# Kernel tuning notes

Measured on AMD Instinct MI355X. Metric: run time of the kernel, lower is better.

Reference implementation:

```python
import jax, jax.numpy as jnp
import numpy as np
import math

DIM = 512
HEADS = 16
HD = DIM // HEADS
HT, WT = 32, 32          # trained input_resolution
LT = HT * WT             # trained_len
TBL = (2 * HT - 1) * (2 * WT - 1)  # 3969 rows in relative_coords_table
CPB_HID = 512


def _l2norm(a, eps=1e-12):
    n = jnp.linalg.norm(a, axis=-1, keepdims=True)
    return a / jnp.maximum(n, eps)


def setup_inputs() -> dict:
    key = jax.random.key(0)
    ks = jax.random.split(key, 10)
    B, N = 8, 1024
    std = 0.02
    return {
        "x": jax.random.normal(ks[0], (B, N, DIM), jnp.float32),
        "qkv_w": jax.random.normal(ks[1], (3 * DIM, DIM), jnp.float32) * std,
        "qkv_b": jnp.zeros((3 * DIM,), jnp.float32),
        "proj_w": jax.random.normal(ks[2], (DIM, DIM), jnp.float32) * std,
        "proj_b": jnp.zeros((DIM,), jnp.float32),
        # softplus-inverse init: softplus(temperature) == 1/0.24
        "temperature": jnp.log(jnp.exp(jnp.ones((HEADS, 1, 1), jnp.float32) / 0.24) - 1.0),
        "query_embedding": jax.random.normal(ks[3], (HEADS, 1, HD), jnp.float32) * 0.02,
        "cpb_fc1_w": jax.random.normal(ks[4], (CPB_HID, 2), jnp.float32) * std,
        "cpb_fc1_b": jnp.zeros((CPB_HID,), jnp.float32),
        "cpb_fc2_w": jax.random.normal(ks[5], (HEADS, CPB_HID), jnp.float32) * std,
        "cpb_fc2_b": jnp.zeros((HEADS,), jnp.float32),
        "relative_coords_table": jax.random.uniform(ks[6], (TBL, 2), jnp.float32, -1.0, 1.0),
        "relative_pos_index": jax.random.randint(ks[7], (LT * LT,), 0, TBL, jnp.int32),
        "seq_length_scale": jnp.float32(math.log(float(N))),
        "padding_mask": jnp.zeros((B, N), bool),
        "H": 32,
        "W": 32,
    }


def reference(x, qkv_w, qkv_b, proj_w, proj_b, temperature, query_embedding,
              cpb_fc1_w, cpb_fc1_b, cpb_fc2_w, cpb_fc2_b,
              relative_coords_table, seq_length_scale,
              relative_pos_index, padding_mask, H, W):
    B, N, C = x.shape
    # qkv projection -> [B, N, 3, heads, hd] -> per-tensor [B, heads, N, hd]
    qkv = (x @ qkv_w.T + qkv_b).reshape(B, N, 3, HEADS, HD)
    q, k, v = (jnp.transpose(qkv[:, :, i], (0, 2, 1, 3)) for i in range(3))

    # continuous position bias MLP: [TBL, 2] -> [TBL, heads]
    t = jnp.maximum(relative_coords_table @ cpb_fc1_w.T + cpb_fc1_b, 0.0)
    t = t @ cpb_fc2_w.T + cpb_fc2_b                       # [TBL, heads]
    rb = t.T[:, relative_pos_index]                       # [heads, LT*LT]
    rb = rb.reshape(HEADS, LT, HT, WT)
    rb = jax.image.resize(rb, (HEADS, LT, H, W), 'bilinear')   # interp key axis
    rb = rb.reshape(HEADS, LT, N).transpose(0, 2, 1).reshape(HEADS, N, HT, WT)
    rb = jax.image.resize(rb, (HEADS, N, H, W), 'bilinear')    # interp query axis
    rb = rb.reshape(HEADS, N, N).transpose(0, 2, 1)             # [heads, N, N]

    scale = jax.nn.softplus(temperature) * seq_length_scale     # [heads, 1, 1]
    qn = (_l2norm(q) + query_embedding[None]) * scale[None]     # [B, heads, N, hd]
    kn = _l2norm(k)
    attn = jnp.einsum('bhnd,bhmd->bhnm', qn, kn) + rb[None]     # [B, heads, N, N]
    attn = jax.nn.softmax(attn, axis=-1)
    out = jnp.einsum('bhnm,bhmd->bhnd', attn, v)
    out = out.transpose(0, 2, 1, 3).reshape(B, N, C)
    return out @ proj_w.T + proj_b
```

## Files before the change

### kernel.cpp

```cpp
#include <hip/hip_runtime.h>
#include <math.h>

#define BATCH 8
#define NSEQ  1024
#define DIMC  512
#define HEADS 16
#define HD    32
#define TBLN  3969
#define QROWS (BATCH*HEADS*NSEQ)
#define LOG2E 1.4426950408889634f

typedef __attribute__((ext_vector_type(8))) short bf16x8;
typedef __attribute__((ext_vector_type(4))) float f32x4;

__device__ __forceinline__ unsigned short f2bf(float f) {
  union { float f; unsigned u; } c; c.f = f;
  unsigned x = c.u + 0x7fffu + ((c.u >> 16) & 1u);
  return (unsigned short)(x >> 16);
}
__device__ __forceinline__ float bf2f(unsigned short h) {
  union { unsigned u; float f; } c; c.u = ((unsigned)h) << 16; return c.f;
}
__device__ __forceinline__ unsigned cvt_pk_bf16(float lo, float hi) {
  unsigned r;
  asm("v_cvt_pk_bf16_f32 %0, %1, %2" : "=v"(r) : "v"(lo), "v"(hi));
  return r;
}

#define GLD(gsrc, ldst) __builtin_amdgcn_global_load_lds( \
      (const __attribute__((address_space(1))) unsigned int*)(gsrc), \
      (__attribute__((address_space(3))) unsigned int*)(ldst), 16, 0, 0)

__global__ __launch_bounds__(256) void split_kernel(
    const float* __restrict__ src, unsigned short* __restrict__ hi,
    unsigned short* __restrict__ lo, int n4)
{
  int gid = blockIdx.x * 256 + threadIdx.x;
  if (gid >= n4) return;
  float4 v = ((const float4*)src)[gid];
  float vv[4] = {v.x, v.y, v.z, v.w};
  unsigned short h[4], l[4];
#pragma unroll
  for (int i = 0; i < 4; ++i) {
    h[i] = f2bf(vv[i]);
    l[i] = f2bf(vv[i] - bf2f(h[i]));
  }
  uint2 hp, lp;
  hp.x = h[0] | ((unsigned)h[1] << 16); hp.y = h[2] | ((unsigned)h[3] << 16);
  lp.x = l[0] | ((unsigned)l[1] << 16); lp.y = l[2] | ((unsigned)l[3] << 16);
  ((uint2*)hi)[gid] = hp;
  ((uint2*)lo)[gid] = lp;
}

template<int EPI>
__global__ __launch_bounds__(256) void gemm_split_kernel(
    const unsigned short* __restrict__ Ah, const unsigned short* __restrict__ Al,
    const unsigned short* __restrict__ Wh, const unsigned short* __restrict__ Wl,
    const float* __restrict__ bias,
    float* __restrict__ o0p, float* __restrict__ o1p, float* __restrict__ o2p)
{
  const int K = DIMC;
  __shared__ __align__(16) unsigned short lds[4 * 4096];
  unsigned short* ldsAh = lds;
  unsigned short* ldsAl = lds + 4096;
  unsigned short* ldsBh = lds + 8192;
  unsigned short* ldsBl = lds + 12288;
  const int tid = threadIdx.x;
  const int wave = tid >> 6, lane = tid & 63;
  const int l16 = lane & 15, hi4 = lane >> 4;
  const int rowBase = blockIdx.y * 128, colBase = blockIdx.x * 128;
  const int warpRow = (wave >> 1) * 64, warpCol = (wave & 1) * 64;

  const int o0 = wave * 2048 + lane * 16;
  const int o1 = o0 + 1024;
  const int row0 = o0 >> 6, s0 = (o0 >> 4) & 3;
  const int row1 = o1 >> 6, s1 = (o1 >> 4) & 3;
  const int g0 = row0 * K + ((s0 ^ ((row0 >> 1) & 3)) << 3);
  const int g1 = row1 * K + ((s1 ^ ((row1 >> 1) & 3)) << 3);

  const unsigned short* A0h = Ah + (size_t)rowBase * K;
  const unsigned short* A0l = Al + (size_t)rowBase * K;
  const unsigned short* W0h = Wh + (size_t)colBase * K;
  const unsigned short* W0l = Wl + (size_t)colBase * K;

  f32x4 acc[4][4] = {};

  float biasv[4];
#pragma unroll
  for (int fj = 0; fj < 4; ++fj)
    biasv[fj] = bias[colBase + warpCol + fj * 16 + l16];

  int ra[4], rbq[4];
#pragma unroll
  for (int f = 0; f < 4; ++f) {
    int rowA = warpRow + f * 16 + l16;
    ra[f] = rowA * 64 + ((hi4 ^ ((rowA >> 1) & 3)) << 4);
    int rowB = warpCol + f * 16 + l16;
    rbq[f] = rowB * 64 + ((hi4 ^ ((rowB >> 1) & 3)) << 4);
  }

  for (int k0 = 0; k0 < K; k0 += 32) {
    __syncthreads();
    GLD(A0h + k0 + g0, (char*)ldsAh + o0);
    GLD(A0h + k0 + g1, (char*)ldsAh + o1);
    GLD(A0l + k0 + g0, (char*)ldsAl + o0);
    GLD(A0l + k0 + g1, (char*)ldsAl + o1);
    GLD(W0h + k0 + g0, (char*)ldsBh + o0);
    GLD(W0h + k0 + g1, (char*)ldsBh + o1);
    GLD(W0l + k0 + g0, (char*)ldsBl + o0);
    GLD(W0l + k0 + g1, (char*)ldsBl + o1);
    __syncthreads();

    bf16x8 a_h[4], a_l[4], b_h[4], b_l[4];
#pragma unroll
    for (int f = 0; f < 4; ++f) {
      a_h[f] = *(const bf16x8*)((const char*)ldsAh + ra[f]);
      a_l[f] = *(const bf16x8*)((const char*)ldsAl + ra[f]);
      b_h[f] = *(const bf16x8*)((const char*)ldsBh + rbq[f]);
      b_l[f] = *(const bf16x8*)((const char*)ldsBl + rbq[f]);
    }
#pragma unroll
    for (int fi = 0; fi < 4; ++fi)
#pragma unroll
      for (int fj = 0; fj < 4; ++fj) {
        acc[fi][fj] = __builtin_amdgcn_mfma_f32_16x16x32_bf16(a_l[fi], b_h[fj], acc[fi][fj], 0, 0, 0);
        acc[fi][fj] = __builtin_amdgcn_mfma_f32_16x16x32_bf16(a_h[fi], b_l[fj], acc[fi][fj], 0, 0, 0);
        acc[fi][fj] = __builtin_amdgcn_mfma_f32_16x16x32_bf16(a_h[fi], b_h[fj], acc[fi][fj], 0, 0, 0);
      }
  }

#pragma unroll
  for (int fi = 0; fi < 4; ++fi)
#pragma unroll
    for (int fj = 0; fj < 4; ++fj)
#pragma unroll
      for (int r = 0; r < 4; ++r) {
        int m = rowBase + warpRow + fi * 16 + hi4 * 4 + r;
        int c = colBase + warpCol + fj * 16 + l16;
        float val = acc[fi][fj][r] + biasv[fj];
        if (EPI == 0) {
          int b = m >> 10, n = m & 1023;
          int which = c >> 9, rem = c & 511;
          int hh = rem >> 5, d = rem & 31;
          float* dst = (which == 0) ? o0p : (which == 1) ? o1p : o2p;
          dst[(((size_t)b * HEADS + hh) * NSEQ + n) * HD + d] = val;
        } else {
          o0p[(size_t)m * DIMC + c] = val;
        }
      }
}

__global__ __launch_bounds__(256) void cpb_kernel(
    const float* __restrict__ table, const float* __restrict__ fc1w,
    const float* __restrict__ fc1b, const float* __restrict__ fc2w,
    const float* __restrict__ fc2b, float* __restrict__ tT)
{
  const int row = blockIdx.x;
  const float c0 = table[row*2], c1 = table[row*2+1];
  __shared__ float hid[512];
  __shared__ float red[256];
  const int tid = threadIdx.x;
  for (int j = tid; j < 512; j += 256)
    hid[j] = fmaxf(fmaf(c0, fc1w[j*2], fmaf(c1, fc1w[j*2+1], fc1b[j])), 0.f);
  __syncthreads();
  const int h = tid & 15, part = tid >> 4;
  float s = 0.f;
#pragma unroll
  for (int jj = 0; jj < 32; ++jj) {
    int j = part*32 + jj;
    s = fmaf(hid[j], fc2w[h*512 + j], s);
  }
  red[tid] = s;
  __syncthreads();
  if (tid < 16) {
    float t = fc2b[tid];
#pragma unroll
    for (int p = 0; p < 16; ++p) t += red[tid + p*16];
    tT[(size_t)tid * TBLN + row] = t;
  }
}

__global__ __launch_bounds__(256) void rb_gather_kernel(
    const float* __restrict__ tT, const int* __restrict__ rpi,
    unsigned short* __restrict__ rbT)
{
  int gid = blockIdx.x * 256 + threadIdx.x;
  int n = gid >> 7, m8 = gid & 127;
  int idx[8];
#pragma unroll
  for (int j = 0; j < 8; ++j) idx[j] = rpi[(size_t)n * NSEQ + m8 * 8 + j];
  const int kt = m8 >> 2, hi4v = m8 & 3;
  const size_t base = (((size_t)0 * 64 + (n >> 4)) * 32 + kt) * 512
                      + ((n & 15) + 16 * hi4v) * 8;
#pragma unroll
  for (int h = 0; h < 16; ++h) {
    bf16x8 v;
#pragma unroll
    for (int j = 0; j < 8; ++j)
      v[j] = (short)f2bf(tT[h * TBLN + idx[j]] * LOG2E);
    *(bf16x8*)(rbT + base + (size_t)h * 64 * 32 * 512) = v;
  }
}

__global__ __launch_bounds__(256) void rowmax_kernel(
    const unsigned short* __restrict__ rbT, float* __restrict__ rbmax)
{
  const int row = blockIdx.x * 4 + (threadIdx.x >> 6);
  const int lane = threadIdx.x & 63;
  const int h = row >> 10, n = row & 1023;
  const int kt = lane >> 1, half = lane & 1;
  const size_t base = (((size_t)h * 64 + (n >> 4)) * 32 + kt) * 512;
  bf16x8 a = *(const bf16x8*)(rbT + base + ((n & 15) + 16 * (2 * half)) * 8);
  bf16x8 b = *(const bf16x8*)(rbT + base + ((n & 15) + 16 * (2 * half + 1)) * 8);
  float m = -1e30f;
#pragma unroll
  for (int j = 0; j < 8; ++j) {
    m = fmaxf(m, bf2f((unsigned short)a[j]));
    m = fmaxf(m, bf2f((unsigned short)b[j]));
  }
#pragma unroll
  for (int s = 32; s >= 1; s >>= 1) m = fmaxf(m, __shfl_xor(m, s));
  if (lane == 0) rbmax[row] = m;
}

__global__ __launch_bounds__(256) void normsplit_kernel(
    const float* __restrict__ qb, const float* __restrict__ kb,
    const float* __restrict__ temperature, const float* __restrict__ qe,
    const float* __restrict__ sls,
    unsigned short* __restrict__ qh, unsigned short* __restrict__ ql,
    unsigned short* __restrict__ khT, unsigned short* __restrict__ klT,
    float* __restrict__ qmag)
{
  const int gid = blockIdx.x * 256 + threadIdx.x;
  const int lane = gid & 31;
  const int row = gid >> 5;
  const bool isQ = row < QROWS;
  const float* src = isQ ? qb : kb;
  const int r = isQ ? row : row - QROWS;
  float x = src[(size_t)r * HD + lane];
  float ss = x * x;
#pragma unroll
  for (int m = 16; m >= 1; m >>= 1) ss += __shfl_xor(ss, m);
  float y = x / fmaxf(sqrtf(ss), 1e-12f);
  if (isQ) {
    const int h = (r >> 10) & (HEADS - 1);
    float scale = log1pf(__expf(temperature[h])) * sls[0];
    y = (y + qe[h * HD + lane]) * scale;
    float s2 = y * y;
#pragma unroll
    for (int m = 16; m >= 1; m >>= 1) s2 += __shfl_xor(s2, m);
    if (lane == 0) qmag[r] = sqrtf(s2);
  }
  unsigned short hi = f2bf(y);
  unsigned short lo = f2bf(y - bf2f(hi));
  if (isQ) {
    size_t idx = (size_t)r * HD + lane;
    qh[idx] = hi; ql[idx] = lo;
  } else {
    const int bh = r >> 10, n = r & 1023;
    const int kt = n >> 5, kr = n & 31;
    const int s = (kr >> 2) & 1;
    const int l16v = 4 * (kr >> 3) + (kr & 3);
    size_t idx = ((((size_t)bh * 32 + kt) * 2 + s) * 512)
                 + (l16v + 16 * (lane >> 3)) * 8 + (lane & 7);
    khT[idx] = hi; klT[idx] = lo;
  }
}

__global__ __launch_bounds__(256) void vt_kernel(
    const float* __restrict__ vb, unsigned short* __restrict__ vtT)
{
  __shared__ float tile[32][257];
  const int bh = blockIdx.x, ch = blockIdx.y;
  const int t = threadIdx.x;
  const float* src = vb + ((size_t)bh * NSEQ + ch * 256) * HD;
#pragma unroll
  for (int i = 0; i < 32; ++i) {
    int idx = i * 256 + t;
    tile[idx & 31][idx >> 5] = src[idx];
  }
  __syncthreads();
  unsigned short* dst = vtT + (size_t)bh * 32 * 2 * 512;
#pragma unroll
  for (int i = 0; i < 32; ++i) {
    int idx = i * 256 + t;
    int d = idx >> 8, nl = idx & 255;
    int n = ch * 256 + nl;
    size_t a = (((size_t)(n >> 5) * 2) + (d >> 4)) * 512
               + ((d & 15) + 16 * ((n >> 3) & 3)) * 8 + (n & 7);
    dst[a] = f2bf(tile[d][nl]);
  }
}

__global__ __launch_bounds__(256, 6) void attn_mfma_kernel(
    const unsigned short* __restrict__ qh, const unsigned short* __restrict__ ql,
    const unsigned short* __restrict__ khT, const unsigned short* __restrict__ klT,
    const unsigned short* __restrict__ vtT, const unsigned short* __restrict__ rbT,
    const float* __restrict__ qmag, const float* __restrict__ rbmax,
    unsigned short* __restrict__ aoh, unsigned short* __restrict__ aol)
{
  const int bh = blockIdx.x;
  const int h = bh & (HEADS - 1), b = bh >> 4;
  const int wave = threadIdx.x >> 6;
  const int lane = threadIdx.x & 63;
  const int l16 = lane & 15, hi4 = lane >> 4;
  const int qbase = blockIdx.y * 64 + wave * 16;

  const int qrow = qbase + l16;
  bf16x8 qhf, qlf;
  {
    size_t ro = ((size_t)bh * NSEQ + qrow) * HD + hi4 * 8;
    qhf = *(const bf16x8*)(qh + ro);
    qlf = *(const bf16x8*)(ql + ro);
  }
  const float Ms = qmag[(size_t)bh * NSEQ + qrow] * (1.01f * LOG2E)
                   + rbmax[h * NSEQ + qrow] + 0.2f;

  bf16x8 ones;
#pragma unroll
  for (int j = 0; j < 8; ++j) ones[j] = (short)0x3f80;

  f32x4 accV0 = {}, accV1 = {}, accL = {};

  const unsigned short* khB = khT + (size_t)bh * 32768 + lane * 8;
  const unsigned short* klB = klT + (size_t)bh * 32768 + lane * 8;
  const unsigned short* vtB = vtT + (size_t)bh * 32768 + lane * 8;
  const unsigned short* rbB = rbT
      + ((size_t)(h * 64 + blockIdx.y * 4 + wave) * 32) * 512 + lane * 8;

  for (int kt = 0; kt < 32; ++kt) {
    bf16x8 kh0 = *(const bf16x8*)(khB + kt * 1024);
    bf16x8 kh1 = *(const bf16x8*)(khB + kt * 1024 + 512);
    bf16x8 kl0 = *(const bf16x8*)(klB + kt * 1024);
    bf16x8 kl1 = *(const bf16x8*)(klB + kt * 1024 + 512);
    bf16x8 vt0 = *(const bf16x8*)(vtB + kt * 1024);
    bf16x8 vt1 = *(const bf16x8*)(vtB + kt * 1024 + 512);
    bf16x8 b8  = *(const bf16x8*)(rbB + kt * 512);

    f32x4 D0 = {0.f, 0.f, 0.f, 0.f};
    f32x4 D1 = {0.f, 0.f, 0.f, 0.f};
    __builtin_amdgcn_s_setprio(1);
    D0 = __builtin_amdgcn_mfma_f32_16x16x32_bf16(kh0, qhf, D0, 0, 0, 0);
    D0 = __builtin_amdgcn_mfma_f32_16x16x32_bf16(kh0, qlf, D0, 0, 0, 0);
    D0 = __builtin_amdgcn_mfma_f32_16x16x32_bf16(kl0, qhf, D0, 0, 0, 0);
    D1 = __builtin_amdgcn_mfma_f32_16x16x32_bf16(kh1, qhf, D1, 0, 0, 0);
    D1 = __builtin_amdgcn_mfma_f32_16x16x32_bf16(kh1, qlf, D1, 0, 0, 0);
    D1 = __builtin_amdgcn_mfma_f32_16x16x32_bf16(kl1, qhf, D1, 0, 0, 0);
    __builtin_amdgcn_s_setprio(0);

    float p0[4], p1[4];
#pragma unroll
    for (int r = 0; r < 4; ++r) {
      float a0 = fmaf(D0[r], LOG2E, bf2f((unsigned short)b8[r]))     - Ms;
      float a1 = fmaf(D1[r], LOG2E, bf2f((unsigned short)b8[4 + r])) - Ms;
      p0[r] = __builtin_amdgcn_exp2f(a0);
      p1[r] = __builtin_amdgcn_exp2f(a1);
    }
    union { bf16x8 v; unsigned u[4]; } pa;
    pa.u[0] = cvt_pk_bf16(p0[0], p0[1]);
    pa.u[1] = cvt_pk_bf16(p0[2], p0[3]);
    pa.u[2] = cvt_pk_bf16(p1[0], p1[1]);
    pa.u[3] = cvt_pk_bf16(p1[2], p1[3]);

    __builtin_amdgcn_s_setprio(1);
    accV0 = __builtin_amdgcn_mfma_f32_16x16x32_bf16(pa.v, vt0, accV0, 0, 0, 0);
    accV1 = __builtin_amdgcn_mfma_f32_16x16x32_bf16(pa.v, vt1, accV1, 0, 0, 0);
    accL  = __builtin_amdgcn_mfma_f32_16x16x32_bf16(pa.v, ones, accL, 0, 0, 0);
    __builtin_amdgcn_s_setprio(0);
  }

#pragma unroll
  for (int r = 0; r < 4; ++r) {
    float inv = 1.f / accL[r];
#pragma unroll
    for (int df = 0; df < 2; ++df) {
      size_t idx = ((size_t)b * NSEQ + qbase + hi4 * 4 + r) * DIMC
                   + h * HD + df * 16 + l16;
      float val = (df ? accV1[r] : accV0[r]) * inv;
      unsigned short hh = f2bf(val);
      aoh[idx] = hh;
      aol[idx] = f2bf(val - bf2f(hh));
    }
  }
}

extern "C" void kernel_launch(void* const* d_in, const int* in_sizes, int n_in,
                              void* d_out, int out_size, void* d_ws, size_t ws_size,
                              hipStream_t stream)
{
  (void)in_sizes; (void)n_in; (void)out_size; (void)ws_size;
  const float* x      = (const float*)d_in[0];
  const float* qkv_w  = (const float*)d_in[1];
  const float* qkv_b  = (const float*)d_in[2];
  const float* proj_w = (const float*)d_in[3];
  const float* proj_b = (const float*)d_in[4];
  const float* temp   = (const float*)d_in[5];
  const float* qe     = (const float*)d_in[6];
  const float* fc1w   = (const float*)d_in[7];
  const float* fc1b   = (const float*)d_in[8];
  const float* fc2w   = (const float*)d_in[9];
  const float* fc2b   = (const float*)d_in[10];
  const float* tbl    = (const float*)d_in[11];
  const int*   rpi    = (const int*)d_in[12];
  const float* sls    = (const float*)d_in[13];

  char* ws = (char*)d_ws;
  const size_t perT = (size_t)BATCH * HEADS * NSEQ * HD;
  float* qb = (float*)ws;
  float* kb = qb + perT;
  float* vb = kb + perT;
  float* tT = vb + perT;
  unsigned short* qh = (unsigned short*)(tT + 65536);
  unsigned short* ql = qh + perT;
  unsigned short* khT = ql + perT;
  unsigned short* klT = khT + perT;
  unsigned short* vtT = klT + perT;
  unsigned short* xh = vtT + perT;
  unsigned short* xl = xh + perT;
  unsigned short* pwh = xl + perT;
  unsigned short* pwl = pwh + 262144;
  float* rbmax = (float*)(pwl + 262144);
  float* qmag  = rbmax + 16384;
  unsigned short* qwh = qh;
  unsigned short* qwl = qh + 786432;
  unsigned short* rbT = (unsigned short*)qb;
  unsigned short* aoh = xh;
  unsigned short* aol = xl;

  split_kernel<<<dim3(4096), 256, 0, stream>>>(x, xh, xl, 1048576);
  split_kernel<<<dim3(768),  256, 0, stream>>>(qkv_w, qwh, qwl, 196608);
  split_kernel<<<dim3(256),  256, 0, stream>>>(proj_w, pwh, pwl, 65536);
  gemm_split_kernel<0><<<dim3(12, 64), 256, 0, stream>>>(
      xh, xl, qwh, qwl, qkv_b, qb, kb, vb);
  cpb_kernel<<<dim3(TBLN), 256, 0, stream>>>(tbl, fc1w, fc1b, fc2w, fc2b, tT);
  normsplit_kernel<<<dim3((2*QROWS*32)/256), 256, 0, stream>>>(
      qb, kb, temp, qe, sls, qh, ql, khT, klT, qmag);
  vt_kernel<<<dim3(BATCH*HEADS, NSEQ/256), 256, 0, stream>>>(vb, vtT);
  rb_gather_kernel<<<dim3((NSEQ*NSEQ/8)/256), 256, 0, stream>>>(tT, rpi, rbT);
  rowmax_kernel<<<dim3(HEADS*NSEQ/4), 256, 0, stream>>>(rbT, rbmax);
  attn_mfma_kernel<<<dim3(BATCH*HEADS, NSEQ/64), 256, 0, stream>>>(
      qh, ql, khT, klT, vtT, rbT, qmag, rbmax, aoh, aol);
  gemm_split_kernel<1><<<dim3(4, 64), 256, 0, stream>>>(
      aoh, aol, pwh, pwl, proj_b, (float*)d_out, nullptr, nullptr);
}
```

Measured before the change: 353.7 us.

## Fuse V transpose/bf16 pack into QKV GEMM epilogue; shrink proj GEMM tile

```diff
diff --git a/kernel.cpp b/kernel.cpp
--- a/kernel.cpp
+++ b/kernel.cpp
@@ -52,75 +52,93 @@
   ((uint2*)lo)[gid] = lp;
 }
 
-template<int EPI>
+template<int EPI, int BM>
 __global__ __launch_bounds__(256) void gemm_split_kernel(
     const unsigned short* __restrict__ Ah, const unsigned short* __restrict__ Al,
     const unsigned short* __restrict__ Wh, const unsigned short* __restrict__ Wl,
     const float* __restrict__ bias,
-    float* __restrict__ o0p, float* __restrict__ o1p, float* __restrict__ o2p)
+    float* __restrict__ o0p, float* __restrict__ o1p,
+    unsigned short* __restrict__ vtp)
 {
   const int K = DIMC;
-  __shared__ __align__(16) unsigned short lds[4 * 4096];
+  constexpr int ASZ = BM * 32;
+  constexpr int FI  = BM / 32;
+  __shared__ __align__(16) unsigned short lds[2 * ASZ + 8192];
   unsigned short* ldsAh = lds;
-  unsigned short* ldsAl = lds + 4096;
-  unsigned short* ldsBh = lds + 8192;
-  unsigned short* ldsBl = lds + 12288;
+  unsigned short* ldsAl = lds + ASZ;
+  unsigned short* ldsBh = lds + 2 * ASZ;
+  unsigned short* ldsBl = lds + 2 * ASZ + 4096;
   const int tid = threadIdx.x;
   const int wave = tid >> 6, lane = tid & 63;
   const int l16 = lane & 15, hi4 = lane >> 4;
-  const int rowBase = blockIdx.y * 128, colBase = blockIdx.x * 128;
-  const int warpRow = (wave >> 1) * 64, warpCol = (wave & 1) * 64;
-
-  const int o0 = wave * 2048 + lane * 16;
-  const int o1 = o0 + 1024;
-  const int row0 = o0 >> 6, s0 = (o0 >> 4) & 3;
-  const int row1 = o1 >> 6, s1 = (o1 >> 4) & 3;
-  const int g0 = row0 * K + ((s0 ^ ((row0 >> 1) & 3)) << 3);
-  const int g1 = row1 * K + ((s1 ^ ((row1 >> 1) & 3)) << 3);
+  const int rowBase = blockIdx.y * BM, colBase = blockIdx.x * 128;
+  const int warpRow = (wave >> 1) * (BM / 2), warpCol = (wave & 1) * 64;
+
+  const int oB0 = wave * 2048 + lane * 16;
+  const int oB1 = oB0 + 1024;
+  const int rB0 = oB0 >> 6, sB0 = (oB0 >> 4) & 3;
+  const int rB1 = oB1 >> 6, sB1 = (oB1 >> 4) & 3;
+  const int gB0 = rB0 * K + ((sB0 ^ ((rB0 >> 1) & 3)) << 3);
+  const int gB1 = rB1 * K + ((sB1 ^ ((rB1 >> 1) & 3)) << 3);
+  const int oA0 = (BM == 128) ? (wave * 2048 + lane * 16)
+                              : (wave * 1024 + lane * 16);
+  const int oA1 = oA0 + 1024;
+  const int rA0 = oA0 >> 6, sA0 = (oA0 >> 4) & 3;
+  const int rA1 = oA1 >> 6, sA1 = (oA1 >> 4) & 3;
+  const int gA0 = rA0 * K + ((sA0 ^ ((rA0 >> 1) & 3)) << 3);
+  const int gA1 = rA1 * K + ((sA1 ^ ((rA1 >> 1) & 3)) << 3);
 
   const unsigned short* A0h = Ah + (size_t)rowBase * K;
   const unsigned short* A0l = Al + (size_t)rowBase * K;
   const unsigned short* W0h = Wh + (size_t)colBase * K;
   const unsigned short* W0l = Wl + (size_t)colBase * K;
 
-  f32x4 acc[4][4] = {};
+  f32x4 acc[FI][4] = {};
 
   float biasv[4];
 #pragma unroll
   for (int fj = 0; fj < 4; ++fj)
     biasv[fj] = bias[colBase + warpCol + fj * 16 + l16];
 
-  int ra[4], rbq[4];
-#pragma unroll
-  for (int f = 0; f < 4; ++f) {
+  int ra[FI], rbq[4];
+#pragma unroll
+  for (int f = 0; f < FI; ++f) {
     int rowA = warpRow + f * 16 + l16;
     ra[f] = rowA * 64 + ((hi4 ^ ((rowA >> 1) & 3)) << 4);
+  }
+#pragma unroll
+  for (int f = 0; f < 4; ++f) {
     int rowB = warpCol + f * 16 + l16;
     rbq[f] = rowB * 64 + ((hi4 ^ ((rowB >> 1) & 3)) << 4);
   }
 
   for (int k0 = 0; k0 < K; k0 += 32) {
     __syncthreads();
-    GLD(A0h + k0 + g0, (char*)ldsAh + o0);
-    GLD(A0h + k0 + g1, (char*)ldsAh + o1);
-    GLD(A0l + k0 + g0, (char*)ldsAl + o0);
-    GLD(A0l + k0 + g1, (char*)ldsAl + o1);
-    GLD(W0h + k0 + g0, (char*)ldsBh + o0);
-    GLD(W0h + k0 + g1, (char*)ldsBh + o1);
-    GLD(W0l + k0 + g0, (char*)ldsBl + o0);
-    GLD(W0l + k0 + g1, (char*)ldsBl + o1);
+    GLD(A0h + k0 + gA0, (char*)ldsAh + oA0);
+    GLD(A0l + k0 + gA0, (char*)ldsAl + oA0);
+    if constexpr (BM == 128) {
+      GLD(A0h + k0 + gA1, (char*)ldsAh + oA1);
+      GLD(A0l + k0 + gA1, (char*)ldsAl + oA1);
+    }
+    GLD(W0h + k0 + gB0, (char*)ldsBh + oB0);
+    GLD(W0h + k0 + gB1, (char*)ldsBh + oB1);
+    GLD(W0l + k0 + gB0, (char*)ldsBl + oB0);
+    GLD(W0l + k0 + gB1, (char*)ldsBl + oB1);
     __syncthreads();
 
-    bf16x8 a_h[4], a_l[4], b_h[4], b_l[4];
-#pragma unroll
-    for (int f = 0; f < 4; ++f) {
+    bf16x8 a_h[FI], a_l[FI], b_h[4], b_l[4];
+#pragma unroll
+    for (int f = 0; f < FI; ++f) {
       a_h[f] = *(const bf16x8*)((const char*)ldsAh + ra[f]);
       a_l[f] = *(const bf16x8*)((const char*)ldsAl + ra[f]);
+    }
+#pragma unroll
+    for (int f = 0; f < 4; ++f) {
       b_h[f] = *(const bf16x8*)((const char*)ldsBh + rbq[f]);
       b_l[f] = *(const bf16x8*)((const char*)ldsBl + rbq[f]);
     }
 #pragma unroll
-    for (int fi = 0; fi < 4; ++fi)
+    for (int fi = 0; fi < FI; ++fi)
 #pragma unroll
       for (int fj = 0; fj < 4; ++fj) {
         acc[fi][fj] = __builtin_amdgcn_mfma_f32_16x16x32_bf16(a_l[fi], b_h[fj], acc[fi][fj], 0, 0, 0);
@@ -130,7 +148,7 @@
   }
 
 #pragma unroll
-  for (int fi = 0; fi < 4; ++fi)
+  for (int fi = 0; fi < FI; ++fi)
 #pragma unroll
     for (int fj = 0; fj < 4; ++fj)
 #pragma unroll
@@ -142,8 +160,16 @@
           int b = m >> 10, n = m & 1023;
           int which = c >> 9, rem = c & 511;
           int hh = rem >> 5, d = rem & 31;
-          float* dst = (which == 0) ? o0p : (which == 1) ? o1p : o2p;
-          dst[(((size_t)b * HEADS + hh) * NSEQ + n) * HD + d] = val;
+          if (which == 2) {
+            int bh = b * HEADS + hh;
+            size_t a = (size_t)bh * 32768
+                     + (size_t)(n >> 5) * 1024 + (size_t)(d >> 4) * 512
+                     + ((d & 15) + 16 * ((n >> 3) & 3)) * 8 + (n & 7);
+            vtp[a] = f2bf(val);
+          } else {
+            float* dst = (which == 0) ? o0p : o1p;
+            dst[(((size_t)b * HEADS + hh) * NSEQ + n) * HD + d] = val;
+          }
         } else {
           o0p[(size_t)m * DIMC + c] = val;
         }
@@ -264,31 +290,6 @@
     size_t idx = ((((size_t)bh * 32 + kt) * 2 + s) * 512)
                  + (l16v + 16 * (lane >> 3)) * 8 + (lane & 7);
     khT[idx] = hi; klT[idx] = lo;
-  }
-}
-
-__global__ __launch_bounds__(256) void vt_kernel(
-    const float* __restrict__ vb, unsigned short* __restrict__ vtT)
-{
-  __shared__ float tile[32][257];
-  const int bh = blockIdx.x, ch = blockIdx.y;
-  const int t = threadIdx.x;
-  const float* src = vb + ((size_t)bh * NSEQ + ch * 256) * HD;
-#pragma unroll
-  for (int i = 0; i < 32; ++i) {
-    int idx = i * 256 + t;
-    tile[idx & 31][idx >> 5] = src[idx];
-  }
-  __syncthreads();
-  unsigned short* dst = vtT + (size_t)bh * 32 * 2 * 512;
-#pragma unroll
-  for (int i = 0; i < 32; ++i) {
-    int idx = i * 256 + t;
-    int d = idx >> 8, nl = idx & 255;
-    int n = ch * 256 + nl;
-    size_t a = (((size_t)(n >> 5) * 2) + (d >> 4)) * 512
-               + ((d & 15) + 16 * ((n >> 3) & 3)) * 8 + (n & 7);
-    dst[a] = f2bf(tile[d][nl]);
   }
 }
 
@@ -430,16 +431,15 @@
   split_kernel<<<dim3(4096), 256, 0, stream>>>(x, xh, xl, 1048576);
   split_kernel<<<dim3(768),  256, 0, stream>>>(qkv_w, qwh, qwl, 196608);
   split_kernel<<<dim3(256),  256, 0, stream>>>(proj_w, pwh, pwl, 65536);
-  gemm_split_kernel<0><<<dim3(12, 64), 256, 0, stream>>>(
-      xh, xl, qwh, qwl, qkv_b, qb, kb, vb);
+  gemm_split_kernel<0, 128><<<dim3(12, 64), 256, 0, stream>>>(
+      xh, xl, qwh, qwl, qkv_b, qb, kb, vtT);
   cpb_kernel<<<dim3(TBLN), 256, 0, stream>>>(tbl, fc1w, fc1b, fc2w, fc2b, tT);
   normsplit_kernel<<<dim3((2*QROWS*32)/256), 256, 0, stream>>>(
       qb, kb, temp, qe, sls, qh, ql, khT, klT, qmag);
-  vt_kernel<<<dim3(BATCH*HEADS, NSEQ/256), 256, 0, stream>>>(vb, vtT);
   rb_gather_kernel<<<dim3((NSEQ*NSEQ/8)/256), 256, 0, stream>>>(tT, rpi, rbT);
   rowmax_kernel<<<dim3(HEADS*NSEQ/4), 256, 0, stream>>>(rbT, rbmax);
   attn_mfma_kernel<<<dim3(BATCH*HEADS, NSEQ/64), 256, 0, stream>>>(
       qh, ql, khT, klT, vtT, rbT, qmag, rbmax, aoh, aol);
-  gemm_split_kernel<1><<<dim3(4, 64), 256, 0, stream>>>(
+  gemm_split_kernel<1, 64><<<dim3(4, 128), 256, 0, stream>>>(
       aoh, aol, pwh, pwl, proj_b, (float*)d_out, nullptr, nullptr);
 }
```

Result: faster. 339.8 us (-3.9%).
